# Optimization experiments

Measured on AMD Instinct MI355X. Metric: run time of the kernel, lower is better.

Reference implementation:

```python
import jax, jax.numpy as jnp
import numpy as np

DIM = 320
HEADS = 8
D_HEAD = 40
CTX_DIM = 768
INNER_FF = 4 * DIM  # 1280
EPS = 1e-5


def _ln(x, w, b):
    mu = jnp.mean(x, axis=-1, keepdims=True)
    var = jnp.mean(jnp.square(x - mu), axis=-1, keepdims=True)
    return (x - mu) * jax.lax.rsqrt(var + EPS) * w + b


def _attn(xq, ctx, Wq, Wk, Wv, Wo, bo):
    # Wq: [dim, inner]; Wk/Wv: [ctx_dim, inner]; Wo: [inner, dim]
    b, n, _ = xq.shape
    m = ctx.shape[1]
    scale = D_HEAD ** -0.5
    q = (xq @ Wq).reshape(b, n, HEADS, D_HEAD)
    k = (ctx @ Wk).reshape(b, m, HEADS, D_HEAD)
    v = (ctx @ Wv).reshape(b, m, HEADS, D_HEAD)
    sim = jnp.einsum('bihd,bjhd->bhij', q, k) * scale
    attn = jax.nn.softmax(sim, axis=-1)
    out = jnp.einsum('bhij,bjhd->bihd', attn, v).reshape(b, n, HEADS * D_HEAD)
    return out @ Wo + bo


def setup_inputs() -> dict:
    key = jax.random.key(0)
    ks = jax.random.split(key, 20)
    s = 0.02
    inner = HEADS * D_HEAD  # 320
    d = {
        'x': jax.random.normal(ks[0], (2, 4096, DIM), jnp.float32),
        'context': jax.random.normal(ks[1], (2, 77, CTX_DIM), jnp.float32),
        # norm params
        'ln1_w': jnp.ones((DIM,)), 'ln1_b': jnp.zeros((DIM,)),
        'ln2_w': jnp.ones((DIM,)), 'ln2_b': jnp.zeros((DIM,)),
        'ln3_w': jnp.ones((DIM,)), 'ln3_b': jnp.zeros((DIM,)),
        # attn1 (self)
        'a1_Wq': jax.random.normal(ks[2], (DIM, inner)) * s,
        'a1_Wk': jax.random.normal(ks[3], (DIM, inner)) * s,
        'a1_Wv': jax.random.normal(ks[4], (DIM, inner)) * s,
        'a1_Wo': jax.random.normal(ks[5], (inner, DIM)) * s,
        'a1_bo': jnp.zeros((DIM,)),
        # attn2 (cross)
        'a2_Wq': jax.random.normal(ks[6], (DIM, inner)) * s,
        'a2_Wk': jax.random.normal(ks[7], (CTX_DIM, inner)) * s,
        'a2_Wv': jax.random.normal(ks[8], (CTX_DIM, inner)) * s,
        'a2_Wo': jax.random.normal(ks[9], (inner, DIM)) * s,
        'a2_bo': jnp.zeros((DIM,)),
        # GEGLU feed-forward
        'ff_W1': jax.random.normal(ks[10], (DIM, 2 * INNER_FF)) * s,
        'ff_b1': jnp.zeros((2 * INNER_FF,)),
        'ff_W2': jax.random.normal(ks[11], (INNER_FF, DIM)) * s,
        'ff_b2': jnp.zeros((DIM,)),
    }
    return d


def reference(x, context, ln1_w, ln1_b, ln2_w, ln2_b, ln3_w, ln3_b,
              a1_Wq, a1_Wk, a1_Wv, a1_Wo, a1_bo,
              a2_Wq, a2_Wk, a2_Wv, a2_Wo, a2_bo,
              ff_W1, ff_b1, ff_W2, ff_b2):
    h = _ln(x, ln1_w, ln1_b)
    x = _attn(h, h, a1_Wq, a1_Wk, a1_Wv, a1_Wo, a1_bo) + x
    h = _ln(x, ln2_w, ln2_b)
    x = _attn(h, context, a2_Wq, a2_Wk, a2_Wv, a2_Wo, a2_bo) + x
    h = _ln(x, ln3_w, ln3_b)
    proj = h @ ff_W1 + ff_b1
    u, gate = jnp.split(proj, 2, axis=-1)
    ff = (u * jax.nn.gelu(gate, approximate=False)) @ ff_W2 + ff_b2
    return ff + x
```

## Files before the change

kernel.cpp:

```cpp
#include <hip/hip_runtime.h>
#include <hip/hip_bf16.h>
#include <math.h>

typedef __hip_bfloat16 bf16;
typedef __attribute__((ext_vector_type(8))) short bf16x8;
typedef __attribute__((ext_vector_type(4))) short bf16x4;
typedef __attribute__((ext_vector_type(4))) float f32x4;
typedef __attribute__((ext_vector_type(2))) unsigned int u32x2;

#define DIM 320
#define HEADS 8
#define DHEAD 40
#define CTXD 768
#define FFI 1280
#define NQ 4096
#define NCTX 77
#define BATCH 2

static __device__ __forceinline__ short f2bs(float v) {
    union { bf16 b; short s; } x; x.b = __float2bfloat16(v); return x.s;
}
static __device__ __forceinline__ float bs2f(short s) {
    return __uint_as_float(((unsigned)(unsigned short)s) << 16);
}
static __device__ __forceinline__ unsigned pkbf(float hi, float lo) {
    return __builtin_amdgcn_perm(__float_as_uint(hi), __float_as_uint(lo), 0x07060302u);
}

__global__ void __launch_bounds__(256) wtrans_all(
    const float* q1s, const float* k1s, const float* v1s, const float* o1s,
    const float* q2s, const float* o2s, const float* k2s, const float* v2s,
    const float* w1s, const float* w2s,
    short* q1d, short* k1d, short* v1d, short* o1d,
    short* q2d, short* o2d, short* k2d, short* v2d,
    short* w1d, short* w2d)
{
    int bid = blockIdx.x;
    const float* W; short* Wt; int K, N, base;
    if (bid < 600) {
        int ws = bid / 100; base = bid % 100; K = DIM; N = DIM;
        W  = ws == 0 ? q1s : ws == 1 ? k1s : ws == 2 ? v1s : ws == 3 ? o1s : ws == 4 ? q2s : o2s;
        Wt = ws == 0 ? q1d : ws == 1 ? k1d : ws == 2 ? v1d : ws == 3 ? o1d : ws == 4 ? q2d : o2d;
    } else if (bid < 1080) {
        int i = bid - 600; int ws = i / 240; base = i % 240; K = CTXD; N = DIM;
        W = ws ? v2s : k2s; Wt = ws ? v2d : k2d;
    } else if (bid < 1880) {
        base = bid - 1080; K = DIM; N = 2 * FFI; W = w1s; Wt = w1d;
    } else {
        base = bid - 1880; K = FFI; N = DIM; W = w2s; Wt = w2d;
    }
    int ntx = N / 32;
    int n0 = (base % ntx) * 32, k0 = (base / ntx) * 32;
    __shared__ float T[32][33];
    int c = threadIdx.x & 31, r8 = threadIdx.x >> 5;
#pragma unroll
    for (int rr = 0; rr < 4; ++rr) {
        int r = r8 + rr * 8;
        T[r][c] = W[(size_t)(k0 + r) * N + n0 + c];
    }
    __syncthreads();
#pragma unroll
    for (int rr = 0; rr < 4; ++rr) {
        int r = r8 + rr * 8;
        Wt[(size_t)(n0 + r) * K + k0 + c] = f2bs(T[c][r]);
    }
}

template<bool SRCB16>
__global__ void __launch_bounds__(256) ln_kernel(const void* __restrict__ srcp,
                          const float* __restrict__ w, const float* __restrict__ bp,
                          short* __restrict__ out, int rows)
{
    int row = blockIdx.x * 4 + (threadIdx.x >> 6);
    int lane = threadIdx.x & 63;
    float v[8];
    float s = 0.f, s2 = 0.f;
    if (lane < 40) {
        if (SRCB16) {
            bf16x8 xv = *(const bf16x8*)((const short*)srcp + (size_t)row * DIM + lane * 8);
#pragma unroll
            for (int j = 0; j < 8; ++j) { v[j] = bs2f(xv[j]); s += v[j]; s2 += v[j] * v[j]; }
        } else {
            const float* rp = (const float*)srcp + (size_t)row * DIM + lane * 8;
#pragma unroll
            for (int j = 0; j < 8; ++j) { v[j] = rp[j]; s += v[j]; s2 += v[j] * v[j]; }
        }
    }
#pragma unroll
    for (int off = 32; off; off >>= 1) { s += __shfl_xor(s, off); s2 += __shfl_xor(s2, off); }
    float mean = s * (1.f / DIM);
    float var = s2 * (1.f / DIM) - mean * mean;
    float rstd = rsqrtf(var + 1e-5f);
    if (lane < 40) {
        bf16x8 ov;
#pragma unroll
        for (int j = 0; j < 8; ++j)
            ov[j] = f2bs((v[j] - mean) * rstd * w[lane * 8 + j] + bp[lane * 8 + j]);
        *(bf16x8*)(out + (size_t)row * DIM + lane * 8) = ov;
    }
}

template<int MODE>
__global__ void __launch_bounds__(256) gemm128(const short* __restrict__ A,
                          const short* __restrict__ Wt,
                          const float* __restrict__ bias,
                          const float* __restrict__ res,
                          short* __restrict__ resb,
                          short* __restrict__ outb,
                          float* __restrict__ outf,
                          int N, int K, float oscale)
{
    __shared__ short As[128 * 72];
    __shared__ short Bs[64 * 72];
    const int tid = threadIdx.x;
    const int w = tid >> 6, lane = tid & 63, lrow = lane & 15, lgrp = lane >> 4;
    const int wr = w >> 1, wc = w & 1;
    const int m0 = blockIdx.y * 128, n0 = blockIdx.x * 64;
    f32x4 acc[4][2] = {};
    for (int k0 = 0; k0 < K; k0 += 64) {
        __syncthreads();
#pragma unroll
        for (int l = 0; l < 4; ++l) {
            int idx = tid + (l << 8);
            int arow = idx >> 3, ac = idx & 7;
            *(bf16x8*)&As[arow * 72 + ac * 8] =
                *(const bf16x8*)(A + (size_t)(m0 + arow) * K + k0 + ac * 8);
        }
#pragma unroll
        for (int l = 0; l < 2; ++l) {
            int idx = tid + (l << 8);
            int brow = idx >> 3, bc = idx & 7;
            *(bf16x8*)&Bs[brow * 72 + bc * 8] =
                *(const bf16x8*)(Wt + (size_t)(n0 + brow) * K + k0 + bc * 8);
        }
        __syncthreads();
#pragma unroll
        for (int s = 0; s < 2; ++s) {
            bf16x8 b0 = *(const bf16x8*)&Bs[(wc * 32 + lrow) * 72 + s * 32 + lgrp * 8];
            bf16x8 b1 = *(const bf16x8*)&Bs[(wc * 32 + 16 + lrow) * 72 + s * 32 + lgrp * 8];
#pragma unroll
            for (int m = 0; m < 4; ++m) {
                bf16x8 a = *(const bf16x8*)&As[(wr * 64 + m * 16 + lrow) * 72 + s * 32 + lgrp * 8];
                acc[m][0] = __builtin_amdgcn_mfma_f32_16x16x32_bf16(a, b0, acc[m][0], 0, 0, 0);
                acc[m][1] = __builtin_amdgcn_mfma_f32_16x16x32_bf16(a, b1, acc[m][1], 0, 0, 0);
            }
        }
    }
#pragma unroll
    for (int n = 0; n < 2; ++n) {
        int col = n0 + wc * 32 + n * 16 + lrow;
        float bvx = bias ? bias[col] : 0.f;
#pragma unroll
        for (int m = 0; m < 4; ++m) {
#pragma unroll
            for (int r = 0; r < 4; ++r) {
                int row = m0 + wr * 64 + m * 16 + lgrp * 4 + r;
                float v = acc[m][n][r] + bvx;
                size_t o = (size_t)row * N + col;
                if (MODE == 0)      outb[o] = f2bs(v * oscale);
                else if (MODE == 1) resb[o] = f2bs(v + res[o]);
                else if (MODE == 2) resb[o] = f2bs(v + bs2f(resb[o]));
                else                outf[o] = v + bs2f(resb[o]);
            }
        }
    }
}

__global__ void __launch_bounds__(256) qkv128(const short* __restrict__ A,
                          const short* __restrict__ wq, const short* __restrict__ wk,
                          const short* __restrict__ wv,
                          short* __restrict__ qb, short* __restrict__ kbuf,
                          short* __restrict__ vts, float qscale)
{
    __shared__ short As[128 * 72];
    __shared__ short Bs[64 * 72];
    const int tid = threadIdx.x;
    const int z = blockIdx.z;
    const short* Wt = z == 0 ? wq : z == 1 ? wk : wv;
    const int w = tid >> 6, lane = tid & 63, lrow = lane & 15, lgrp = lane >> 4;
    const int wr = w >> 1, wc = w & 1;
    const int m0 = blockIdx.y * 128, n0 = blockIdx.x * 64;
    f32x4 acc[4][2] = {};
    for (int k0 = 0; k0 < DIM; k0 += 64) {
        __syncthreads();
#pragma unroll
        for (int l = 0; l < 4; ++l) {
            int idx = tid + (l << 8);
            int arow = idx >> 3, ac = idx & 7;
            *(bf16x8*)&As[arow * 72 + ac * 8] =
                *(const bf16x8*)(A + (size_t)(m0 + arow) * DIM + k0 + ac * 8);
        }
#pragma unroll
        for (int l = 0; l < 2; ++l) {
            int idx = tid + (l << 8);
            int brow = idx >> 3, bc = idx & 7;
            *(bf16x8*)&Bs[brow * 72 + bc * 8] =
                *(const bf16x8*)(Wt + (size_t)(n0 + brow) * DIM + k0 + bc * 8);
        }
        __syncthreads();
#pragma unroll
        for (int s = 0; s < 2; ++s) {
            bf16x8 b0 = *(const bf16x8*)&Bs[(wc * 32 + lrow) * 72 + s * 32 + lgrp * 8];
            bf16x8 b1 = *(const bf16x8*)&Bs[(wc * 32 + 16 + lrow) * 72 + s * 32 + lgrp * 8];
#pragma unroll
            for (int m = 0; m < 4; ++m) {
                bf16x8 a = *(const bf16x8*)&As[(wr * 64 + m * 16 + lrow) * 72 + s * 32 + lgrp * 8];
                acc[m][0] = __builtin_amdgcn_mfma_f32_16x16x32_bf16(a, b0, acc[m][0], 0, 0, 0);
                acc[m][1] = __builtin_amdgcn_mfma_f32_16x16x32_bf16(a, b1, acc[m][1], 0, 0, 0);
            }
        }
    }
#pragma unroll
    for (int n = 0; n < 2; ++n) {
        int col = n0 + wc * 32 + n * 16 + lrow;
#pragma unroll
        for (int m = 0; m < 4; ++m) {
            if (z == 2) {
                int row0 = m0 + wr * 64 + m * 16 + lgrp * 4;
                int b_ = row0 >> 12, kv = row0 & (NQ - 1);
                int hh = col / DHEAD, d = col - hh * DHEAD;
                bf16x4 pv;
#pragma unroll
                for (int r = 0; r < 4; ++r) pv[r] = f2bs(acc[m][n][r]);
                *(bf16x4*)(vts + (size_t)((b_ * HEADS + hh) * 48 + d) * NQ + kv) = pv;
            } else {
#pragma unroll
                for (int r = 0; r < 4; ++r) {
                    int row = m0 + wr * 64 + m * 16 + lgrp * 4 + r;
                    float v = acc[m][n][r];
                    if (z == 0) qb[(size_t)row * DIM + col] = f2bs(v * qscale);
                    else        kbuf[(size_t)row * DIM + col] = f2bs(v);
                }
            }
        }
    }
}

__global__ void __launch_bounds__(256) geglu128(const short* __restrict__ A,
                           const short* __restrict__ Wt1,
                           const float* __restrict__ b1, short* __restrict__ G)
{
    __shared__ short As[128 * 72];
    __shared__ short Bu[64 * 72];
    __shared__ short Bg[64 * 72];
    const int tid = threadIdx.x;
    const int w = tid >> 6, lane = tid & 63, lrow = lane & 15, lgrp = lane >> 4;
    const int wr = w >> 1, wc = w & 1;
    const int m0 = blockIdx.y * 128, n0 = blockIdx.x * 64;
    f32x4 au[4][2] = {}, ag[4][2] = {};
    for (int k0 = 0; k0 < DIM; k0 += 64) {
        __syncthreads();
#pragma unroll
        for (int l = 0; l < 4; ++l) {
            int idx = tid + (l << 8);
            int arow = idx >> 3, ac = idx & 7;
            *(bf16x8*)&As[arow * 72 + ac * 8] =
                *(const bf16x8*)(A + (size_t)(m0 + arow) * DIM + k0 + ac * 8);
        }
#pragma unroll
        for (int l = 0; l < 2; ++l) {
            int idx = tid + (l << 8);
            int brow = idx >> 3, bc = idx & 7;
            *(bf16x8*)&Bu[brow * 72 + bc * 8] =
                *(const bf16x8*)(Wt1 + (size_t)(n0 + brow) * DIM + k0 + bc * 8);
            *(bf16x8*)&Bg[brow * 72 + bc * 8] =
                *(const bf16x8*)(Wt1 + (size_t)(FFI + n0 + brow) * DIM + k0 + bc * 8);
        }
        __syncthreads();
#pragma unroll
        for (int s = 0; s < 2; ++s) {
            bf16x8 bu0 = *(const bf16x8*)&Bu[(wc * 32 + lrow) * 72 + s * 32 + lgrp * 8];
            bf16x8 bu1 = *(const bf16x8*)&Bu[(wc * 32 + 16 + lrow) * 72 + s * 32 + lgrp * 8];
            bf16x8 bg0 = *(const bf16x8*)&Bg[(wc * 32 + lrow) * 72 + s * 32 + lgrp * 8];
            bf16x8 bg1 = *(const bf16x8*)&Bg[(wc * 32 + 16 + lrow) * 72 + s * 32 + lgrp * 8];
#pragma unroll
            for (int m = 0; m < 4; ++m) {
                bf16x8 a = *(const bf16x8*)&As[(wr * 64 + m * 16 + lrow) * 72 + s * 32 + lgrp * 8];
                au[m][0] = __builtin_amdgcn_mfma_f32_16x16x32_bf16(a, bu0, au[m][0], 0, 0, 0);
                au[m][1] = __builtin_amdgcn_mfma_f32_16x16x32_bf16(a, bu1, au[m][1], 0, 0, 0);
                ag[m][0] = __builtin_amdgcn_mfma_f32_16x16x32_bf16(a, bg0, ag[m][0], 0, 0, 0);
                ag[m][1] = __builtin_amdgcn_mfma_f32_16x16x32_bf16(a, bg1, ag[m][1], 0, 0, 0);
            }
        }
    }
#pragma unroll
    for (int n = 0; n < 2; ++n) {
        int col = n0 + wc * 32 + n * 16 + lrow;
        float bu = b1[col], bg = b1[FFI + col];
#pragma unroll
        for (int m = 0; m < 4; ++m) {
#pragma unroll
            for (int r = 0; r < 4; ++r) {
                int row = m0 + wr * 64 + m * 16 + lgrp * 4 + r;
                float u = au[m][n][r] + bu;
                float g = ag[m][n][r] + bg;
                float gelu = 0.5f * g * (1.f + erff(g * 0.70710678f));
                G[(size_t)row * FFI + col] = f2bs(u * gelu);
            }
        }
    }
}

__global__ void __launch_bounds__(256) mfma_crosskv(const float* __restrict__ ctx,
                          const short* __restrict__ wk2, const short* __restrict__ wv2,
                          short* __restrict__ k2, short* __restrict__ vt2)
{
    __shared__ short As[64 * 72];
    __shared__ short Bs[64 * 72];
    const int tid = threadIdx.x;
    const int z = blockIdx.z;
    const short* Wt = z ? wv2 : wk2;
    const int Mc = BATCH * NCTX;
    const int w = tid >> 6, lane = tid & 63, lrow = lane & 15, lgrp = lane >> 4;
    const int m0 = blockIdx.y * 64, n0 = blockIdx.x * 64;
    f32x4 acc[4] = {};
    for (int kb = 0; kb < CTXD / 64; ++kb) {
        const int k0 = kb << 6;
        __syncthreads();
#pragma unroll
        for (int l = 0; l < 2; ++l) {
            int idx = tid + (l << 8);
            int arow = idx >> 3, ac = idx & 7;
            int grow = m0 + arow;
            bf16x8 v = {};
            if (grow < Mc) {
                const float* Af = ctx + (size_t)grow * CTXD + k0 + ac * 8;
#pragma unroll
                for (int j = 0; j < 8; ++j) v[j] = f2bs(Af[j]);
            }
            *(bf16x8*)&As[arow * 72 + ac * 8] = v;
            *(bf16x8*)&Bs[arow * 72 + ac * 8] =
                *(const bf16x8*)(Wt + (size_t)(n0 + arow) * CTXD + k0 + ac * 8);
        }
        __syncthreads();
#pragma unroll
        for (int s = 0; s < 2; ++s) {
            bf16x8 a = *(const bf16x8*)&As[(w * 16 + lrow) * 72 + s * 32 + lgrp * 8];
#pragma unroll
            for (int ct = 0; ct < 4; ++ct) {
                bf16x8 b = *(const bf16x8*)&Bs[(ct * 16 + lrow) * 72 + s * 32 + lgrp * 8];
                acc[ct] = __builtin_amdgcn_mfma_f32_16x16x32_bf16(a, b, acc[ct], 0, 0, 0);
            }
        }
    }
#pragma unroll
    for (int ct = 0; ct < 4; ++ct) {
        int col = n0 + ct * 16 + lrow;
#pragma unroll
        for (int r = 0; r < 4; ++r) {
            int row = m0 + w * 16 + lgrp * 4 + r;
            if (row >= Mc) continue;
            float v = acc[ct][r];
            if (z == 0) k2[(size_t)row * DIM + col] = f2bs(v);
            else {
                int b_ = row / NCTX, kv = row - b_ * NCTX;
                int hh = col / DHEAD, d = col - hh * DHEAD;
                vt2[(size_t)((b_ * HEADS + hh) * 48 + d) * 128 + kv] = f2bs(v);
            }
        }
    }
}

template<bool FULL>
__global__ void __launch_bounds__(512) flash_mfma(const short* __restrict__ Q,
                           const short* __restrict__ Kb,
                           const short* __restrict__ VtG,
                           short* __restrict__ O,
                           int kvlen, int kvs)
{
    __shared__ short Ks[2][64 * 64];
    __shared__ short Vt[2][48 * 64];
    __shared__ short Ps[128 * 64];
    const int tid = threadIdx.x;
    const int w = tid >> 6, lane = tid & 63, lrow = lane & 15, lgrp = lane >> 4;
    const int hh = blockIdx.y, b = blockIdx.z;
    const int q0 = blockIdx.x * 128;
    const int swz = (lrow & 7) << 4;

    if (tid < 512) { ((bf16x8*)Ks[0])[tid] = (bf16x8){}; ((bf16x8*)Ks[1])[tid] = (bf16x8){}; }
    if (tid < 384) {
        short fill = ((tid >> 3) == 40) ? (short)0x3F80 : (short)0;
        bf16x8 f8 = {fill, fill, fill, fill, fill, fill, fill, fill};
        ((bf16x8*)Vt[0])[tid] = f8; ((bf16x8*)Vt[1])[tid] = f8;
    }

    const size_t qbase = ((size_t)(b * NQ + q0 + w * 16 + lrow)) * DIM + hh * DHEAD;
    bf16x8 bq0 = *(const bf16x8*)(Q + qbase + lgrp * 8);
    bf16x8 bq1 = {};
    if (lgrp == 0) bq1 = *(const bf16x8*)(Q + qbase + 32);

    const bool isK = tid < 320;
    const int kv0 = isK ? tid / 5 : 0, cc0 = isK ? tid % 5 : 0;
    const int vc0 = tid - 320;
    const int vd0 = vc0 >> 3, vcc0 = vc0 & 7;
    const bool hasV1 = tid < 192;
    const int vd1 = (192 + tid) >> 3, vcc1 = (192 + tid) & 7;
    const bool wrV1 = hasV1 && (vd1 < DHEAD);

    bf16x8 st0, st1;
    const size_t kbase = (size_t)b * kvlen;
    const size_t vbase = (size_t)((b * HEADS + hh) * 48);

    auto issue = [&](int t) {
        const int j0 = t << 6;
        if (isK)
            st0 = *(const bf16x8*)(Kb + (kbase + j0 + kv0) * DIM + hh * DHEAD + cc0 * 8);
        else
            st0 = *(const bf16x8*)(VtG + (vbase + vd0) * kvs + j0 + vcc0 * 8);
        if (wrV1)
            st1 = *(const bf16x8*)(VtG + (vbase + vd1) * kvs + j0 + vcc1 * 8);
    };
    auto commit = [&](int bi) {
        if (isK)
            *(bf16x8*)((char*)Ks[bi] + kv0 * 128 + ((cc0 * 16) ^ ((kv0 & 7) << 4))) = st0;
        else
            *(bf16x8*)((char*)Vt[bi] + vd0 * 128 + ((vcc0 * 16) ^ ((vd0 & 7) << 4))) = st0;
        if (wrV1)
            *(bf16x8*)((char*)Vt[bi] + vd1 * 128 + ((vcc1 * 16) ^ ((vd1 & 7) << 4))) = st1;
    };

    f32x4 o_acc[3] = {};

    issue(0);
    __syncthreads();
    commit(0);
    const int ntiles = (kvlen + 63) >> 6;
    char* prow = (char*)Ps + (w * 16 + lrow) * 128;
    for (int t = 0; t < ntiles; ++t) {
        const int j0 = t << 6;
        const int bi = t & 1;
        if (t + 1 < ntiles) issue(t + 1);
        __syncthreads();

        f32x4 sacc[4] = {};
        __builtin_amdgcn_s_setprio(1);
#pragma unroll
        for (int ct = 0; ct < 4; ++ct) {
            const char* krow = (char*)Ks[bi] + (ct * 16 + lrow) * 128;
            bf16x8 ak0 = *(const bf16x8*)(krow + ((lgrp * 16) ^ swz));
            sacc[ct] = __builtin_amdgcn_mfma_f32_16x16x32_bf16(ak0, bq0, sacc[ct], 0, 0, 0);
            bf16x8 ak1 = *(const bf16x8*)(krow + ((64 + lgrp * 16) ^ swz));
            sacc[ct] = __builtin_amdgcn_mfma_f32_16x16x32_bf16(ak1, bq1, sacc[ct], 0, 0, 0);
        }
        __builtin_amdgcn_s_setprio(0);
        if (!FULL && j0 + 64 > kvlen) {
#pragma unroll
            for (int ct = 0; ct < 4; ++ct)
#pragma unroll
                for (int r = 0; r < 4; ++r)
                    if (j0 + ct * 16 + lgrp * 4 + r >= kvlen) sacc[ct][r] = -1e30f;
        }
#pragma unroll
        for (int ct = 0; ct < 4; ++ct) {
            float p0 = __builtin_amdgcn_exp2f(sacc[ct][0]);
            float p1 = __builtin_amdgcn_exp2f(sacc[ct][1]);
            float p2 = __builtin_amdgcn_exp2f(sacc[ct][2]);
            float p3 = __builtin_amdgcn_exp2f(sacc[ct][3]);
            u32x2 pk; pk[0] = pkbf(p1, p0); pk[1] = pkbf(p3, p2);
            *(u32x2*)(prow + ((ct * 32 + lgrp * 8) ^ swz)) = pk;
        }
        __builtin_amdgcn_s_setprio(1);
#pragma unroll
        for (int s = 0; s < 2; ++s) {
            bf16x8 bp = *(const bf16x8*)(prow + ((s * 64 + lgrp * 16) ^ swz));
#pragma unroll
            for (int dt = 0; dt < 3; ++dt) {
                bf16x8 av = *(const bf16x8*)((char*)Vt[bi] + (dt * 16 + lrow) * 128 + ((s * 64 + lgrp * 16) ^ swz));
                o_acc[dt] = __builtin_amdgcn_mfma_f32_16x16x32_bf16(av, bp, o_acc[dt], 0, 0, 0);
            }
        }
        __builtin_amdgcn_s_setprio(0);
        if (t + 1 < ntiles) commit((t + 1) & 1);
    }
    float lsum = __shfl(o_acc[2][0], 32 + (lane & 15));
    float invl = 1.f / lsum;
    const size_t obase = ((size_t)(b * NQ + q0 + w * 16 + lrow)) * DIM + hh * DHEAD;
#pragma unroll
    for (int dt = 0; dt < 3; ++dt) {
        int dbase = dt * 16 + lgrp * 4;
        if (dbase < DHEAD) {
            u32x2 ov;
            ov[0] = pkbf(o_acc[dt][1] * invl, o_acc[dt][0] * invl);
            ov[1] = pkbf(o_acc[dt][3] * invl, o_acc[dt][2] * invl);
            *(u32x2*)(O + obase + dbase) = ov;
        }
    }
}

extern "C" void kernel_launch(void* const* d_in, const int* in_sizes, int n_in,
                              void* d_out, int out_size, void* d_ws, size_t ws_size,
                              hipStream_t stream)
{
    const float* x      = (const float*)d_in[0];
    const float* ctx    = (const float*)d_in[1];
    const float* ln1_w  = (const float*)d_in[2];
    const float* ln1_b  = (const float*)d_in[3];
    const float* ln2_w  = (const float*)d_in[4];
    const float* ln2_b  = (const float*)d_in[5];
    const float* ln3_w  = (const float*)d_in[6];
    const float* ln3_b  = (const float*)d_in[7];
    const float* a1_Wq  = (const float*)d_in[8];
    const float* a1_Wk  = (const float*)d_in[9];
    const float* a1_Wv  = (const float*)d_in[10];
    const float* a1_Wo  = (const float*)d_in[11];
    const float* a1_bo  = (const float*)d_in[12];
    const float* a2_Wq  = (const float*)d_in[13];
    const float* a2_Wk  = (const float*)d_in[14];
    const float* a2_Wv  = (const float*)d_in[15];
    const float* a2_Wo  = (const float*)d_in[16];
    const float* a2_bo  = (const float*)d_in[17];
    const float* ff_W1  = (const float*)d_in[18];
    const float* ff_b1  = (const float*)d_in[19];
    const float* ff_W2  = (const float*)d_in[20];
    const float* ff_b2  = (const float*)d_in[21];

    const int M = BATCH * NQ;
    const float qscale2 = (float)(0.15811388300841898 * 1.4426950408889634);

    char* p = (char*)d_ws;
    auto carve = [&](size_t bytes) { char* r = p; p += (bytes + 255) & ~255ULL; return r; };
    short* h       = (short*)carve((size_t)M * DIM * 2);
    short* qb      = (short*)carve((size_t)M * DIM * 2);
    short* kbuf    = (short*)carve((size_t)M * DIM * 2);
    short* attnout = (short*)carve((size_t)M * DIM * 2);
    short* resb    = (short*)carve((size_t)M * DIM * 2);
    short* gbuf    = (short*)carve((size_t)M * FFI * 2);
    short* VtS     = (short*)carve((size_t)BATCH * HEADS * 48 * NQ * 2);
    short* Vt2     = (short*)carve((size_t)BATCH * HEADS * 48 * 128 * 2);
    short* k2      = (short*)carve((size_t)256 * DIM * 2);
    short* wtq1    = (short*)carve((size_t)DIM * DIM * 2);
    short* wtk1    = (short*)carve((size_t)DIM * DIM * 2);
    short* wtv1    = (short*)carve((size_t)DIM * DIM * 2);
    short* wto1    = (short*)carve((size_t)DIM * DIM * 2);
    short* wtq2    = (short*)carve((size_t)DIM * DIM * 2);
    short* wto2    = (short*)carve((size_t)DIM * DIM * 2);
    short* wtk2    = (short*)carve((size_t)DIM * CTXD * 2);
    short* wtv2    = (short*)carve((size_t)DIM * CTXD * 2);
    short* wt1     = (short*)carve((size_t)2 * FFI * DIM * 2);
    short* wt2     = (short*)carve((size_t)DIM * FFI * 2);

    dim3 blk(256);
    dim3 g128(DIM / 64, M / 128);
    dim3 gattn(NQ / 128, HEADS, BATCH);

    wtrans_all<<<2280, blk, 0, stream>>>(a1_Wq, a1_Wk, a1_Wv, a1_Wo, a2_Wq, a2_Wo,
                                         a2_Wk, a2_Wv, ff_W1, ff_W2,
                                         wtq1, wtk1, wtv1, wto1, wtq2, wto2,
                                         wtk2, wtv2, wt1, wt2);
    ln_kernel<false><<<M / 4, blk, 0, stream>>>(x, ln1_w, ln1_b, h, M);
    qkv128<<<dim3(5, 64, 3), blk, 0, stream>>>(h, wtq1, wtk1, wtv1, qb, kbuf, VtS, qscale2);
    flash_mfma<true><<<gattn, dim3(512), 0, stream>>>(qb, kbuf, VtS, attnout, NQ, NQ);
    gemm128<1><<<g128, blk, 0, stream>>>(attnout, wto1, a1_bo, x, resb, nullptr, nullptr, DIM, DIM, 1.f);
    ln_kernel<true><<<M / 4, blk, 0, stream>>>(resb, ln2_w, ln2_b, h, M);
    gemm128<0><<<g128, blk, 0, stream>>>(h, wtq2, nullptr, nullptr, nullptr, qb, nullptr, DIM, DIM, qscale2);
    mfma_crosskv<<<dim3(5, 3, 2), blk, 0, stream>>>(ctx, wtk2, wtv2, k2, Vt2);
    flash_mfma<false><<<gattn, dim3(512), 0, stream>>>(qb, k2, Vt2, attnout, NCTX, 128);
    gemm128<2><<<g128, blk, 0, stream>>>(attnout, wto2, a2_bo, nullptr, resb, nullptr, nullptr, DIM, DIM, 1.f);
    ln_kernel<true><<<M / 4, blk, 0, stream>>>(resb, ln3_w, ln3_b, h, M);
    geglu128<<<dim3(FFI / 64, M / 128), blk, 0, stream>>>(h, wt1, ff_b1, gbuf);
    gemm128<3><<<g128, blk, 0, stream>>>(gbuf, wt2, ff_b2, nullptr, resb, nullptr, (float*)d_out, DIM, FFI, 1.f);
}
```

Baseline: 236.2 us.

## Process two 16-row query subtiles per wave in flash attention with 256 threads

The flash attention kernel now runs 4 waves of 256 threads per block instead of 8, and each wave handles 32 query rows as two 16-row subtiles that share the K and V fragments read from LDS. K/V tile loading is redistributed across the smaller thread count, with up to three vector loads per thread. The aim is to halve LDS reads of K/V per MFMA and the number of waves that sync on each barrier. The cost is roughly double the accumulator registers per wave, which may lower occupancy, and fewer waves available to hide latency.

```diff
diff --git a/kernel.cpp b/kernel.cpp
--- a/kernel.cpp
+++ b/kernel.cpp
@@ -362,7 +362,7 @@
 }
 
 template<bool FULL>
-__global__ void __launch_bounds__(512) flash_mfma(const short* __restrict__ Q,
+__global__ void __launch_bounds__(256) flash_mfma(const short* __restrict__ Q,
                            const short* __restrict__ Kb,
                            const short* __restrict__ VtG,
                            short* __restrict__ O,
@@ -377,70 +377,76 @@
     const int q0 = blockIdx.x * 128;
     const int swz = (lrow & 7) << 4;
 
-    if (tid < 512) { ((bf16x8*)Ks[0])[tid] = (bf16x8){}; ((bf16x8*)Ks[1])[tid] = (bf16x8){}; }
-    if (tid < 384) {
-        short fill = ((tid >> 3) == 40) ? (short)0x3F80 : (short)0;
+    for (int i = tid; i < 1024; i += 256) ((bf16x8*)Ks)[i] = (bf16x8){};
+    for (int i = tid; i < 768; i += 256) {
+        short fill = (((i % 384) >> 3) == 40) ? (short)0x3F80 : (short)0;
         bf16x8 f8 = {fill, fill, fill, fill, fill, fill, fill, fill};
-        ((bf16x8*)Vt[0])[tid] = f8; ((bf16x8*)Vt[1])[tid] = f8;
-    }
-
-    const size_t qbase = ((size_t)(b * NQ + q0 + w * 16 + lrow)) * DIM + hh * DHEAD;
-    bf16x8 bq0 = *(const bf16x8*)(Q + qbase + lgrp * 8);
-    bf16x8 bq1 = {};
-    if (lgrp == 0) bq1 = *(const bf16x8*)(Q + qbase + 32);
-
-    const bool isK = tid < 320;
-    const int kv0 = isK ? tid / 5 : 0, cc0 = isK ? tid % 5 : 0;
-    const int vc0 = tid - 320;
-    const int vd0 = vc0 >> 3, vcc0 = vc0 & 7;
-    const bool hasV1 = tid < 192;
-    const int vd1 = (192 + tid) >> 3, vcc1 = (192 + tid) & 7;
-    const bool wrV1 = hasV1 && (vd1 < DHEAD);
-
-    bf16x8 st0, st1;
+        ((bf16x8*)Vt)[i] = f8;
+    }
+
+    const size_t qra = (size_t)(b * NQ + q0 + w * 32 + lrow) * DIM + hh * DHEAD;
+    const size_t qrb = qra + (size_t)16 * DIM;
+    bf16x8 bq0a = *(const bf16x8*)(Q + qra + lgrp * 8);
+    bf16x8 bq0b = *(const bf16x8*)(Q + qrb + lgrp * 8);
+    bf16x8 bq1a = {}, bq1b = {};
+    if (lgrp == 0) {
+        bq1a = *(const bf16x8*)(Q + qra + 32);
+        bq1b = *(const bf16x8*)(Q + qrb + 32);
+    }
+
+    const int kv0 = tid / 5, cc0 = tid % 5;
+    const bool isK1 = tid < 64;
+    const int kv1 = (256 + tid) / 5, cc1 = (256 + tid) % 5;
+    const int vd1 = (tid - 64) >> 3, vcc1 = (tid - 64) & 7;
+    const bool hasV2 = tid < 128;
+    const int vd2 = (192 + tid) >> 3, vcc2 = (192 + tid) & 7;
+
+    bf16x8 st0, st1, st2;
     const size_t kbase = (size_t)b * kvlen;
     const size_t vbase = (size_t)((b * HEADS + hh) * 48);
 
     auto issue = [&](int t) {
         const int j0 = t << 6;
-        if (isK)
-            st0 = *(const bf16x8*)(Kb + (kbase + j0 + kv0) * DIM + hh * DHEAD + cc0 * 8);
-        else
-            st0 = *(const bf16x8*)(VtG + (vbase + vd0) * kvs + j0 + vcc0 * 8);
-        if (wrV1)
-            st1 = *(const bf16x8*)(VtG + (vbase + vd1) * kvs + j0 + vcc1 * 8);
+        st0 = *(const bf16x8*)(Kb + (kbase + j0 + kv0) * DIM + hh * DHEAD + cc0 * 8);
+        if (isK1) st1 = *(const bf16x8*)(Kb + (kbase + j0 + kv1) * DIM + hh * DHEAD + cc1 * 8);
+        else      st1 = *(const bf16x8*)(VtG + (vbase + vd1) * kvs + j0 + vcc1 * 8);
+        if (hasV2) st2 = *(const bf16x8*)(VtG + (vbase + vd2) * kvs + j0 + vcc2 * 8);
     };
     auto commit = [&](int bi) {
-        if (isK)
-            *(bf16x8*)((char*)Ks[bi] + kv0 * 128 + ((cc0 * 16) ^ ((kv0 & 7) << 4))) = st0;
+        *(bf16x8*)((char*)Ks[bi] + kv0 * 128 + ((cc0 * 16) ^ ((kv0 & 7) << 4))) = st0;
+        if (isK1)
+            *(bf16x8*)((char*)Ks[bi] + kv1 * 128 + ((cc1 * 16) ^ ((kv1 & 7) << 4))) = st1;
         else
-            *(bf16x8*)((char*)Vt[bi] + vd0 * 128 + ((vcc0 * 16) ^ ((vd0 & 7) << 4))) = st0;
-        if (wrV1)
             *(bf16x8*)((char*)Vt[bi] + vd1 * 128 + ((vcc1 * 16) ^ ((vd1 & 7) << 4))) = st1;
+        if (hasV2)
+            *(bf16x8*)((char*)Vt[bi] + vd2 * 128 + ((vcc2 * 16) ^ ((vd2 & 7) << 4))) = st2;
     };
 
-    f32x4 o_acc[3] = {};
+    f32x4 oa[3] = {}, ob[3] = {};
 
     issue(0);
     __syncthreads();
     commit(0);
     const int ntiles = (kvlen + 63) >> 6;
-    char* prow = (char*)Ps + (w * 16 + lrow) * 128;
+    char* prow_a = (char*)Ps + (w * 32 + lrow) * 128;
+    char* prow_b = prow_a + 16 * 128;
     for (int t = 0; t < ntiles; ++t) {
         const int j0 = t << 6;
         const int bi = t & 1;
         if (t + 1 < ntiles) issue(t + 1);
         __syncthreads();
 
-        f32x4 sacc[4] = {};
+        f32x4 sa[4] = {}, sb[4] = {};
         __builtin_amdgcn_s_setprio(1);
 #pragma unroll
         for (int ct = 0; ct < 4; ++ct) {
             const char* krow = (char*)Ks[bi] + (ct * 16 + lrow) * 128;
             bf16x8 ak0 = *(const bf16x8*)(krow + ((lgrp * 16) ^ swz));
-            sacc[ct] = __builtin_amdgcn_mfma_f32_16x16x32_bf16(ak0, bq0, sacc[ct], 0, 0, 0);
             bf16x8 ak1 = *(const bf16x8*)(krow + ((64 + lgrp * 16) ^ swz));
-            sacc[ct] = __builtin_amdgcn_mfma_f32_16x16x32_bf16(ak1, bq1, sacc[ct], 0, 0, 0);
+            sa[ct] = __builtin_amdgcn_mfma_f32_16x16x32_bf16(ak0, bq0a, sa[ct], 0, 0, 0);
+            sb[ct] = __builtin_amdgcn_mfma_f32_16x16x32_bf16(ak0, bq0b, sb[ct], 0, 0, 0);
+            sa[ct] = __builtin_amdgcn_mfma_f32_16x16x32_bf16(ak1, bq1a, sa[ct], 0, 0, 0);
+            sb[ct] = __builtin_amdgcn_mfma_f32_16x16x32_bf16(ak1, bq1b, sb[ct], 0, 0, 0);
         }
         __builtin_amdgcn_s_setprio(0);
         if (!FULL && j0 + 64 > kvlen) {
@@ -448,41 +454,52 @@
             for (int ct = 0; ct < 4; ++ct)
 #pragma unroll
                 for (int r = 0; r < 4; ++r)
-                    if (j0 + ct * 16 + lgrp * 4 + r >= kvlen) sacc[ct][r] = -1e30f;
+                    if (j0 + ct * 16 + lgrp * 4 + r >= kvlen) { sa[ct][r] = -1e30f; sb[ct][r] = -1e30f; }
         }
 #pragma unroll
         for (int ct = 0; ct < 4; ++ct) {
-            float p0 = __builtin_amdgcn_exp2f(sacc[ct][0]);
-            float p1 = __builtin_amdgcn_exp2f(sacc[ct][1]);
-            float p2 = __builtin_amdgcn_exp2f(sacc[ct][2]);
-            float p3 = __builtin_amdgcn_exp2f(sacc[ct][3]);
-            u32x2 pk; pk[0] = pkbf(p1, p0); pk[1] = pkbf(p3, p2);
-            *(u32x2*)(prow + ((ct * 32 + lgrp * 8) ^ swz)) = pk;
+            float a0 = __builtin_amdgcn_exp2f(sa[ct][0]);
+            float a1 = __builtin_amdgcn_exp2f(sa[ct][1]);
+            float a2 = __builtin_amdgcn_exp2f(sa[ct][2]);
+            float a3 = __builtin_amdgcn_exp2f(sa[ct][3]);
+            u32x2 pka; pka[0] = pkbf(a1, a0); pka[1] = pkbf(a3, a2);
+            *(u32x2*)(prow_a + ((ct * 32 + lgrp * 8) ^ swz)) = pka;
+            float b0 = __builtin_amdgcn_exp2f(sb[ct][0]);
+            float b1 = __builtin_amdgcn_exp2f(sb[ct][1]);
+            float b2 = __builtin_amdgcn_exp2f(sb[ct][2]);
+            float b3 = __builtin_amdgcn_exp2f(sb[ct][3]);
+            u32x2 pkb; pkb[0] = pkbf(b1, b0); pkb[1] = pkbf(b3, b2);
+            *(u32x2*)(prow_b + ((ct * 32 + lgrp * 8) ^ swz)) = pkb;
         }
         __builtin_amdgcn_s_setprio(1);
 #pragma unroll
         for (int s = 0; s < 2; ++s) {
-            bf16x8 bp = *(const bf16x8*)(prow + ((s * 64 + lgrp * 16) ^ swz));
+            bf16x8 bpa = *(const bf16x8*)(prow_a + ((s * 64 + lgrp * 16) ^ swz));
+            bf16x8 bpb = *(const bf16x8*)(prow_b + ((s * 64 + lgrp * 16) ^ swz));
 #pragma unroll
             for (int dt = 0; dt < 3; ++dt) {
                 bf16x8 av = *(const bf16x8*)((char*)Vt[bi] + (dt * 16 + lrow) * 128 + ((s * 64 + lgrp * 16) ^ swz));
-                o_acc[dt] = __builtin_amdgcn_mfma_f32_16x16x32_bf16(av, bp, o_acc[dt], 0, 0, 0);
+                oa[dt] = __builtin_amdgcn_mfma_f32_16x16x32_bf16(av, bpa, oa[dt], 0, 0, 0);
+                ob[dt] = __builtin_amdgcn_mfma_f32_16x16x32_bf16(av, bpb, ob[dt], 0, 0, 0);
             }
         }
         __builtin_amdgcn_s_setprio(0);
         if (t + 1 < ntiles) commit((t + 1) & 1);
     }
-    float lsum = __shfl(o_acc[2][0], 32 + (lane & 15));
-    float invl = 1.f / lsum;
-    const size_t obase = ((size_t)(b * NQ + q0 + w * 16 + lrow)) * DIM + hh * DHEAD;
+    float la = __shfl(oa[2][0], 32 + lrow);
+    float lb = __shfl(ob[2][0], 32 + lrow);
+    float ia = 1.f / la, ib = 1.f / lb;
 #pragma unroll
     for (int dt = 0; dt < 3; ++dt) {
         int dbase = dt * 16 + lgrp * 4;
         if (dbase < DHEAD) {
-            u32x2 ov;
-            ov[0] = pkbf(o_acc[dt][1] * invl, o_acc[dt][0] * invl);
-            ov[1] = pkbf(o_acc[dt][3] * invl, o_acc[dt][2] * invl);
-            *(u32x2*)(O + obase + dbase) = ov;
+            u32x2 ova, ovb;
+            ova[0] = pkbf(oa[dt][1] * ia, oa[dt][0] * ia);
+            ova[1] = pkbf(oa[dt][3] * ia, oa[dt][2] * ia);
+            *(u32x2*)(O + qra + dbase) = ova;
+            ovb[0] = pkbf(ob[dt][1] * ib, ob[dt][0] * ib);
+            ovb[1] = pkbf(ob[dt][3] * ib, ob[dt][2] * ib);
+            *(u32x2*)(O + qrb + dbase) = ovb;
         }
     }
 }
@@ -549,12 +566,12 @@
                                          wtk2, wtv2, wt1, wt2);
     ln_kernel<false><<<M / 4, blk, 0, stream>>>(x, ln1_w, ln1_b, h, M);
     qkv128<<<dim3(5, 64, 3), blk, 0, stream>>>(h, wtq1, wtk1, wtv1, qb, kbuf, VtS, qscale2);
-    flash_mfma<true><<<gattn, dim3(512), 0, stream>>>(qb, kbuf, VtS, attnout, NQ, NQ);
+    flash_mfma<true><<<gattn, blk, 0, stream>>>(qb, kbuf, VtS, attnout, NQ, NQ);
     gemm128<1><<<g128, blk, 0, stream>>>(attnout, wto1, a1_bo, x, resb, nullptr, nullptr, DIM, DIM, 1.f);
     ln_kernel<true><<<M / 4, blk, 0, stream>>>(resb, ln2_w, ln2_b, h, M);
     gemm128<0><<<g128, blk, 0, stream>>>(h, wtq2, nullptr, nullptr, nullptr, qb, nullptr, DIM, DIM, qscale2);
     mfma_crosskv<<<dim3(5, 3, 2), blk, 0, stream>>>(ctx, wtk2, wtv2, k2, Vt2);
-    flash_mfma<false><<<gattn, dim3(512), 0, stream>>>(qb, k2, Vt2, attnout, NCTX, 128);
+    flash_mfma<false><<<gattn, blk, 0, stream>>>(qb, k2, Vt2, attnout, NCTX, 128);
     gemm128<2><<<g128, blk, 0, stream>>>(attnout, wto2, a2_bo, nullptr, resb, nullptr, nullptr, DIM, DIM, 1.f);
     ln_kernel<true><<<M / 4, blk, 0, stream>>>(resb, ln3_w, ln3_b, h, M);
     geglu128<<<dim3(FFI / 64, M / 128), blk, 0, stream>>>(h, wt1, ff_b1, gbuf);
```

Result: no change. 233.9 us (-1.0%).
